# Performance work log

Measured on AMD Instinct MI355X. Metric: run time of the kernel, lower is better.

Reference implementation:

```python
import jax, jax.numpy as jnp
import numpy as np

N_NODES = 10000   # graph_size1 == graph_size2 (coarse graph nodes)
AS1 = 8           # arr_size1 (input block size)
AS2 = 8           # arr_size2 (output block size)
E = 320000        # number of coarse edges
B = 32            # batch
SIZE1 = N_NODES * AS1
SIZE2 = N_NODES * AS2


def setup_inputs() -> dict:
    key = jax.random.key(0)
    k1, k2, k3, k4 = jax.random.split(key, 4)
    x = jax.random.normal(k1, (B, SIZE1, 1), dtype=jnp.float32)
    indices = jax.random.randint(k2, (2, E), 0, N_NODES, dtype=jnp.int32)
    # torch init: uniform_(0,1) on values (the second uniform_ overwrote the first)
    values = jax.random.uniform(k3, (E, AS1, AS2), dtype=jnp.float32)  # v[e,i,j]
    inv = 1.0 / (E * AS1 * AS2)
    b = jax.random.uniform(k4, (SIZE2,), dtype=jnp.float32, minval=-inv, maxval=inv)
    return {"x": x, "values": values, "b": b, "indices": indices}


def reference(x, values, b, indices):
    # Expanded sparse entry: A[t0*AS2 + j, t1*AS1 + i] = values[e, i, j]
    # => out_block[t0, j] += sum_i values[e,i,j] * x_block[t1, i]
    rows = indices[0]  # output coarse node per edge
    cols = indices[1]  # input coarse node per edge
    xb = x.reshape(B, N_NODES, AS1)          # view input as coarse blocks
    xg = xb[:, cols, :]                      # (B, E, AS1) irregular gather
    contrib = jnp.einsum('bei,eij->bej', xg, values)  # (B, E, AS2)
    out = jax.ops.segment_sum(contrib.transpose(1, 0, 2), rows,
                              num_segments=N_NODES)   # (N_NODES, B, AS2)
    out = out.transpose(1, 0, 2).reshape(B, SIZE2, 1)
    return out + b[None, :, None]
```

## Files before the change

kernel.cpp:

```cpp
#include <hip/hip_runtime.h>
#include <stddef.h>

#define N_NODES 10000
#define NE 320000
#define NB 32
#define SIZE1 80000
#define SIZE2 80000
#define CAP 96

#define WS_CURSOR  0
#define WS_COLS    10000
#define WS_XT      970000
#define WS_VCSR    2250000

typedef short short8 __attribute__((ext_vector_type(8)));
typedef float floatx4 __attribute__((ext_vector_type(4)));
union FragU { short8 v; ushort us[8]; uint4 u4; };

__device__ inline ushort f2bf(float f) {
  union { float f; unsigned u; } c; c.f = f;
  unsigned u = c.u;
  u += 0x7fffu + ((u >> 16) & 1u);
  return (ushort)(u >> 16);
}

__global__ __launch_bounds__(256) void scatter_fused_kernel(const float* __restrict__ x,
                                                            const float* __restrict__ vals,
                                                            const int* __restrict__ idxs,
                                                            int* __restrict__ cursor,
                                                            int* __restrict__ cols_csr,
                                                            ushort* __restrict__ vcsr,
                                                            ushort* __restrict__ xt) {
  const int t = threadIdx.x;
  const int lane = t & 63;
  const int e = blockIdx.x * 256 + t;
  {
    const int r = idxs[e];
    const int c = idxs[NE + e];
    int pos = atomicAdd(&cursor[r], 1);
    int slot = r * CAP + pos;
    const bool ok = pos < CAP;
    if (ok) cols_csr[slot] = c;

    const int ebase = e - lane;
    const int kk = lane >> 3;
    const int j = lane & 7;
#pragma unroll
    for (int it = 0; it < 8; ++it) {
      const int k = it * 8 + kk;
      const int sk = __shfl(slot, k);
      const int okk = __shfl((int)ok, k);
      const float* vp = vals + (size_t)(ebase + k) * 64 + j;
      FragU f;
#pragma unroll
      for (int i = 0; i < 8; ++i) f.us[i] = f2bf(vp[i * 8]);
      if (okk) *(uint4*)(vcsr + (size_t)sk * 64 + j * 8) = f.u4;
    }
  }

  if (blockIdx.x >= 313) return;
  __shared__ float s[32 * 260];
  const int n0 = blockIdx.x * 32;
#pragma unroll
  for (int it = 0; it < 8; ++it) {
    int idx = it * 256 + t;
    int b = idx >> 6, q = idx & 63;
    int base = n0 * 8 + q * 4;
    float4 v = make_float4(0.f, 0.f, 0.f, 0.f);
    if (base < SIZE1) v = *(const float4*)&x[(size_t)b * SIZE1 + base];
    *(float4*)&s[b * 260 + q * 4] = v;
  }
  __syncthreads();
#pragma unroll
  for (int r = 0; r < 4; ++r) {
    int p = r * 256 + t;
    int nl = p >> 5, b = p & 31;
    int n = n0 + nl;
    if (n < N_NODES) {
      FragU f;
      const float* row = &s[b * 260 + nl * 8];
#pragma unroll
      for (int i = 0; i < 8; ++i) f.us[i] = f2bf(row[i]);
      *(uint4*)&xt[(size_t)n * 256 + b * 8] = f.u4;
    }
  }
}

__global__ __launch_bounds__(256) void gather_mfma_kernel(const ushort* __restrict__ xt,
                                                          const ushort* __restrict__ vcsr,
                                                          const float* __restrict__ bias,
                                                          const int* __restrict__ cursor,
                                                          const int* __restrict__ cols_csr,
                                                          float* __restrict__ out) {
  __shared__ float red[3][64][9];
  const int t = threadIdx.x;
  const int lane = t & 63;
  const int w = t >> 6;
  const int n = blockIdx.x;
  const int quad = lane >> 4;
  const int nn = lane & 15;
  const int deg = min(cursor[n], CAP);
  const size_t nbase = (size_t)n * CAP;

  floatx4 acc0 = {0.f, 0.f, 0.f, 0.f};
  floatx4 acc1 = {0.f, 0.f, 0.f, 0.f};

  for (int base = 0; base < deg; base += 64) {
    const int lim = min(64, deg - base);
    int cv = cols_csr[nbase + min(base + lane, deg - 1)];
    const int nslots = (lim + 3) >> 2;

    for (int s0 = w; s0 < nslots; s0 += 8) {
      FragU alo0, ahi0, b0, alo1, ahi1, b1;
      {
        const int le = s0 * 4 + quad;
        const int lec = min(le, lim - 1);
        const int px = __shfl(cv, lec);
        const bool valid = le < lim;
        const ushort* xr = xt + (size_t)px * 256;
        alo0.u4 = *(const uint4*)(xr + nn * 8);
        ahi0.u4 = *(const uint4*)(xr + (16 + nn) * 8);
        b0.u4 = make_uint4(0, 0, 0, 0);
        if (nn < 8 && valid)
          b0.u4 = *(const uint4*)(vcsr + (nbase + base + le) * 64 + nn * 8);
      }
      {
        const int le = (s0 + 4) * 4 + quad;
        const int lec = min(le, lim - 1);
        const int px = __shfl(cv, lec);
        const bool valid = le < lim;
        const ushort* xr = xt + (size_t)px * 256;
        alo1.u4 = *(const uint4*)(xr + nn * 8);
        ahi1.u4 = *(const uint4*)(xr + (16 + nn) * 8);
        b1.u4 = make_uint4(0, 0, 0, 0);
        if (nn < 8 && valid)
          b1.u4 = *(const uint4*)(vcsr + (nbase + base + le) * 64 + nn * 8);
      }
      acc0 = __builtin_amdgcn_mfma_f32_16x16x32_bf16(alo0.v, b0.v, acc0, 0, 0, 0);
      acc1 = __builtin_amdgcn_mfma_f32_16x16x32_bf16(ahi0.v, b0.v, acc1, 0, 0, 0);
      acc0 = __builtin_amdgcn_mfma_f32_16x16x32_bf16(alo1.v, b1.v, acc0, 0, 0, 0);
      acc1 = __builtin_amdgcn_mfma_f32_16x16x32_bf16(ahi1.v, b1.v, acc1, 0, 0, 0);
    }
  }

  if (w > 0) {
#pragma unroll
    for (int r = 0; r < 4; ++r) {
      red[w - 1][lane][r] = acc0[r];
      red[w - 1][lane][4 + r] = acc1[r];
    }
  }
  __syncthreads();
  if (w == 0) {
#pragma unroll
    for (int j = 0; j < 3; ++j)
#pragma unroll
      for (int r = 0; r < 4; ++r) {
        acc0[r] += red[j][lane][r];
        acc1[r] += red[j][lane][4 + r];
      }
    if (nn < 8) {
      float bz = bias[n * 8 + nn];
#pragma unroll
      for (int r = 0; r < 4; ++r) {
        out[(size_t)(quad * 4 + r) * SIZE2 + n * 8 + nn] = acc0[r] + bz;
        out[(size_t)(16 + quad * 4 + r) * SIZE2 + n * 8 + nn] = acc1[r] + bz;
      }
    }
  }
}

extern "C" void kernel_launch(void* const* d_in, const int* in_sizes, int n_in,
                              void* d_out, int out_size, void* d_ws, size_t ws_size,
                              hipStream_t stream) {
  const float* x    = (const float*)d_in[0];
  const float* vals = (const float*)d_in[1];
  const float* bias = (const float*)d_in[2];
  const int*   idxs = (const int*)d_in[3];
  float* out = (float*)d_out;

  int* ws = (int*)d_ws;
  int* cursor    = ws + WS_CURSOR;
  int* cols_csr  = ws + WS_COLS;
  ushort* xt     = (ushort*)(ws + WS_XT);
  ushort* vcsr   = (ushort*)(ws + WS_VCSR);

  hipMemsetAsync(cursor, 0, N_NODES * sizeof(int), stream);

  const int egrid = NE / 256;
  scatter_fused_kernel<<<egrid, 256, 0, stream>>>(x, vals, idxs, cursor, cols_csr, vcsr, xt);
  gather_mfma_kernel<<<N_NODES, 256, 0, stream>>>(xt, vcsr, bias, cursor, cols_csr, out);
}
```

Before: 196.5 us.

## Read edge values directly in gather kernel and assign one wave per node

```diff
diff --git a/kernel.cpp b/kernel.cpp
--- a/kernel.cpp
+++ b/kernel.cpp
@@ -8,10 +8,9 @@
 #define SIZE2 80000
 #define CAP 96
 
-#define WS_CURSOR  0
-#define WS_COLS    10000
-#define WS_XT      970000
-#define WS_VCSR    2250000
+#define WS_CURSOR 0
+#define WS_RECS   10000
+#define WS_XT     1930000
 
 typedef short short8 __attribute__((ext_vector_type(8)));
 typedef float floatx4 __attribute__((ext_vector_type(4)));
@@ -24,79 +23,41 @@
   return (ushort)(u >> 16);
 }
 
-__global__ __launch_bounds__(256) void scatter_fused_kernel(const float* __restrict__ x,
-                                                            const float* __restrict__ vals,
-                                                            const int* __restrict__ idxs,
-                                                            int* __restrict__ cursor,
-                                                            int* __restrict__ cols_csr,
-                                                            ushort* __restrict__ vcsr,
-                                                            ushort* __restrict__ xt) {
+__global__ __launch_bounds__(256) void build_kernel(const float* __restrict__ x,
+                                                    const int* __restrict__ idxs,
+                                                    int* __restrict__ cursor,
+                                                    unsigned long long* __restrict__ recs,
+                                                    ushort* __restrict__ xt) {
   const int t = threadIdx.x;
-  const int lane = t & 63;
   const int e = blockIdx.x * 256 + t;
-  {
-    const int r = idxs[e];
-    const int c = idxs[NE + e];
-    int pos = atomicAdd(&cursor[r], 1);
-    int slot = r * CAP + pos;
-    const bool ok = pos < CAP;
-    if (ok) cols_csr[slot] = c;
+  const int r = idxs[e];
+  const int c = idxs[NE + e];
+  const int pos = atomicAdd(&cursor[r], 1);
+  if (pos < CAP)
+    recs[(size_t)r * CAP + pos] = (unsigned long long)(unsigned)e |
+                                  ((unsigned long long)(unsigned)c << 32);
 
-    const int ebase = e - lane;
-    const int kk = lane >> 3;
-    const int j = lane & 7;
-#pragma unroll
-    for (int it = 0; it < 8; ++it) {
-      const int k = it * 8 + kk;
-      const int sk = __shfl(slot, k);
-      const int okk = __shfl((int)ok, k);
-      const float* vp = vals + (size_t)(ebase + k) * 64 + j;
-      FragU f;
-#pragma unroll
-      for (int i = 0; i < 8; ++i) f.us[i] = f2bf(vp[i * 8]);
-      if (okk) *(uint4*)(vcsr + (size_t)sk * 64 + j * 8) = f.u4;
-    }
-  }
-
-  if (blockIdx.x >= 313) return;
-  __shared__ float s[32 * 260];
-  const int n0 = blockIdx.x * 32;
-#pragma unroll
-  for (int it = 0; it < 8; ++it) {
-    int idx = it * 256 + t;
-    int b = idx >> 6, q = idx & 63;
-    int base = n0 * 8 + q * 4;
-    float4 v = make_float4(0.f, 0.f, 0.f, 0.f);
-    if (base < SIZE1) v = *(const float4*)&x[(size_t)b * SIZE1 + base];
-    *(float4*)&s[b * 260 + q * 4] = v;
-  }
-  __syncthreads();
-#pragma unroll
-  for (int r = 0; r < 4; ++r) {
-    int p = r * 256 + t;
-    int nl = p >> 5, b = p & 31;
-    int n = n0 + nl;
-    if (n < N_NODES) {
-      FragU f;
-      const float* row = &s[b * 260 + nl * 8];
-#pragma unroll
-      for (int i = 0; i < 8; ++i) f.us[i] = f2bf(row[i]);
-      *(uint4*)&xt[(size_t)n * 256 + b * 8] = f.u4;
-    }
-  }
+  const int n = e >> 5;
+  const int b = e & 31;
+  const float* xp = x + (size_t)b * SIZE1 + n * 8;
+  float4 v0 = *(const float4*)xp;
+  float4 v1 = *(const float4*)(xp + 4);
+  FragU f;
+  f.us[0] = f2bf(v0.x); f.us[1] = f2bf(v0.y); f.us[2] = f2bf(v0.z); f.us[3] = f2bf(v0.w);
+  f.us[4] = f2bf(v1.x); f.us[5] = f2bf(v1.y); f.us[6] = f2bf(v1.z); f.us[7] = f2bf(v1.w);
+  *(uint4*)(xt + (size_t)n * 256 + b * 8) = f.u4;
 }
 
 __global__ __launch_bounds__(256) void gather_mfma_kernel(const ushort* __restrict__ xt,
-                                                          const ushort* __restrict__ vcsr,
+                                                          const float* __restrict__ vals,
                                                           const float* __restrict__ bias,
                                                           const int* __restrict__ cursor,
-                                                          const int* __restrict__ cols_csr,
+                                                          const unsigned long long* __restrict__ recs,
                                                           float* __restrict__ out) {
-  __shared__ float red[3][64][9];
   const int t = threadIdx.x;
   const int lane = t & 63;
   const int w = t >> 6;
-  const int n = blockIdx.x;
+  const int n = blockIdx.x * 4 + w;
   const int quad = lane >> 4;
   const int nn = lane & 15;
   const int deg = min(cursor[n], CAP);
@@ -107,34 +68,42 @@
 
   for (int base = 0; base < deg; base += 64) {
     const int lim = min(64, deg - base);
-    int cv = cols_csr[nbase + min(base + lane, deg - 1)];
+    const unsigned long long rv = recs[nbase + base + min(lane, lim - 1)];
+    const int elo = (int)(unsigned)rv;
+    const int ehi = (int)(unsigned)(rv >> 32);
     const int nslots = (lim + 3) >> 2;
 
-    for (int s0 = w; s0 < nslots; s0 += 8) {
+    for (int s = 0; s < nslots; s += 2) {
       FragU alo0, ahi0, b0, alo1, ahi1, b1;
       {
-        const int le = s0 * 4 + quad;
+        const int le = s * 4 + quad;
         const int lec = min(le, lim - 1);
-        const int px = __shfl(cv, lec);
-        const bool valid = le < lim;
+        const int eid = __shfl(elo, lec);
+        const int px  = __shfl(ehi, lec);
         const ushort* xr = xt + (size_t)px * 256;
         alo0.u4 = *(const uint4*)(xr + nn * 8);
-        ahi0.u4 = *(const uint4*)(xr + (16 + nn) * 8);
+        ahi0.u4 = *(const uint4*)(xr + 128 + nn * 8);
         b0.u4 = make_uint4(0, 0, 0, 0);
-        if (nn < 8 && valid)
-          b0.u4 = *(const uint4*)(vcsr + (nbase + base + le) * 64 + nn * 8);
+        if (nn < 8 && le < lim) {
+          const float* vp = vals + (size_t)eid * 64 + nn;
+#pragma unroll
+          for (int i = 0; i < 8; ++i) b0.us[i] = f2bf(vp[i * 8]);
+        }
       }
       {
-        const int le = (s0 + 4) * 4 + quad;
+        const int le = (s + 1) * 4 + quad;
         const int lec = min(le, lim - 1);
-        const int px = __shfl(cv, lec);
-        const bool valid = le < lim;
+        const int eid = __shfl(elo, lec);
+        const int px  = __shfl(ehi, lec);
         const ushort* xr = xt + (size_t)px * 256;
         alo1.u4 = *(const uint4*)(xr + nn * 8);
-        ahi1.u4 = *(const uint4*)(xr + (16 + nn) * 8);
+        ahi1.u4 = *(const uint4*)(xr + 128 + nn * 8);
         b1.u4 = make_uint4(0, 0, 0, 0);
-        if (nn < 8 && valid)
-          b1.u4 = *(const uint4*)(vcsr + (nbase + base + le) * 64 + nn * 8);
+        if (nn < 8 && le < lim) {
+          const float* vp = vals + (size_t)eid * 64 + nn;
+#pragma unroll
+          for (int i = 0; i < 8; ++i) b1.us[i] = f2bf(vp[i * 8]);
+        }
       }
       acc0 = __builtin_amdgcn_mfma_f32_16x16x32_bf16(alo0.v, b0.v, acc0, 0, 0, 0);
       acc1 = __builtin_amdgcn_mfma_f32_16x16x32_bf16(ahi0.v, b0.v, acc1, 0, 0, 0);
@@ -143,29 +112,12 @@
     }
   }
 
-  if (w > 0) {
+  if (nn < 8) {
+    const float bz = bias[n * 8 + nn];
 #pragma unroll
     for (int r = 0; r < 4; ++r) {
-      red[w - 1][lane][r] = acc0[r];
-      red[w - 1][lane][4 + r] = acc1[r];
-    }
-  }
-  __syncthreads();
-  if (w == 0) {
-#pragma unroll
-    for (int j = 0; j < 3; ++j)
-#pragma unroll
-      for (int r = 0; r < 4; ++r) {
-        acc0[r] += red[j][lane][r];
-        acc1[r] += red[j][lane][4 + r];
-      }
-    if (nn < 8) {
-      float bz = bias[n * 8 + nn];
-#pragma unroll
-      for (int r = 0; r < 4; ++r) {
-        out[(size_t)(quad * 4 + r) * SIZE2 + n * 8 + nn] = acc0[r] + bz;
-        out[(size_t)(16 + quad * 4 + r) * SIZE2 + n * 8 + nn] = acc1[r] + bz;
-      }
+      out[(size_t)(quad * 4 + r) * SIZE2 + n * 8 + nn] = acc0[r] + bz;
+      out[(size_t)(16 + quad * 4 + r) * SIZE2 + n * 8 + nn] = acc1[r] + bz;
     }
   }
 }
@@ -180,14 +132,12 @@
   float* out = (float*)d_out;
 
   int* ws = (int*)d_ws;
-  int* cursor    = ws + WS_CURSOR;
-  int* cols_csr  = ws + WS_COLS;
-  ushort* xt     = (ushort*)(ws + WS_XT);
-  ushort* vcsr   = (ushort*)(ws + WS_VCSR);
+  int* cursor = ws + WS_CURSOR;
+  unsigned long long* recs = (unsigned long long*)(ws + WS_RECS);
+  ushort* xt = (ushort*)(ws + WS_XT);
 
   hipMemsetAsync(cursor, 0, N_NODES * sizeof(int), stream);
 
-  const int egrid = NE / 256;
-  scatter_fused_kernel<<<egrid, 256, 0, stream>>>(x, vals, idxs, cursor, cols_csr, vcsr, xt);
-  gather_mfma_kernel<<<N_NODES, 256, 0, stream>>>(xt, vcsr, bias, cursor, cols_csr, out);
+  build_kernel<<<NE / 256, 256, 0, stream>>>(x, idxs, cursor, recs, xt);
+  gather_mfma_kernel<<<N_NODES / 4, 256, 0, stream>>>(xt, vals, bias, cursor, recs, out);
 }
```

New measurement: 178.7 us. 9.0% less time.
